# Kernel tuning notes

Measured on AMD Instinct MI355X. Metric: run time of the kernel, lower is better.

## Reference

```python
import jax, jax.numpy as jnp
import numpy as np

QMIN, QMAX = 0, 255        # 8-bit asymmetric activation quant bounds
GROUP_SIZE = 128

def setup_inputs() -> dict:
    key = jax.random.key(0)
    k1, k2, k3, k4, k5 = jax.random.split(key, 5)
    x = jax.random.normal(k1, (1, 2048, 4096), dtype=jnp.float32)
    qweight = jax.random.randint(k2, (4096, 32, 128), 0, 16, dtype=jnp.int32)  # uint4 codes
    w_scales = jax.random.uniform(k3, (4096, 32), dtype=jnp.float32, minval=0.001, maxval=0.02)
    w_zero_points = jax.random.randint(k4, (4096, 32), 0, 16, dtype=jnp.int32)
    bias = jax.random.normal(k5, (4096,), dtype=jnp.float32)
    return {"x": x, "qweight": qweight, "w_scales": w_scales,
            "w_zero_points": w_zero_points, "bias": bias}

def reference(x, qweight, w_scales, w_zero_points, bias):
    xf = x.astype(jnp.float32)
    # per-token (last-dim) asymmetric dynamic activation quantization
    xmin = jnp.min(xf, axis=-1, keepdims=True)
    xmax = jnp.max(xf, axis=-1, keepdims=True)
    x_scale = jnp.clip((xmax - xmin) / (QMAX - QMIN), 1e-5, None)
    x_zp = jnp.clip(jnp.round(-xmin / x_scale), QMIN, QMAX)
    q = jnp.clip(jnp.round(xf / x_scale) + x_zp, QMIN, QMAX)
    centered_x = (q - x_zp).reshape(*x.shape[:-1], -1, GROUP_SIZE)  # [B,S,G,C]
    # grouped weight dequant (zero-point centered)
    centered_w = qweight.astype(jnp.float32) - w_zero_points.astype(jnp.float32)[..., None]  # [O,G,C]
    acc = jnp.einsum('bsgc,ogc->bsog', centered_x, centered_w)  # [B,S,O,G]
    out = (acc * w_scales[None, None]).sum(axis=-1)  # apply per-group weight scales
    out = out * x_scale  # per-token activation scale
    out = out + bias
    return out
```

## Files before the change

### kernel.cpp

```cpp
#include <hip/hip_runtime.h>
#include <stdint.h>

#define M_DIM 2048
#define N_DIM 4096
#define K_DIM 4096
#define NGROUP 32
#define GSIZE 128

#define RQ_UP   (127.0f / 15.0f)
#define RQ_DOWN (15.0f / 127.0f)

#define BM 256
#define BN 128
#define KSLICE 64
#define NSLICE (K_DIM / KSLICE)
#define ASLOT (BM * KSLICE)
#define BSLOT (BN * KSLICE)

typedef __attribute__((ext_vector_type(4))) int int32x4_t;

static __device__ __forceinline__ void gl2lds16(const void* g, void* l) {
    auto gp = (const __attribute__((address_space(1))) unsigned int*)(uintptr_t)g;
    auto lp = (__attribute__((address_space(3))) unsigned int*)(uintptr_t)l;
    __builtin_amdgcn_global_load_lds(gp, lp, 16, 0, 0);
}

#define WAITVM_(N) asm volatile("s_waitcnt vmcnt(" #N ")" ::: "memory")
#define WAITVM(N) WAITVM_(N)
#define BARRIER() asm volatile("s_barrier" ::: "memory")

#define QUANT_BLOCKS M_DIM
#define DEQ_BLOCKS ((N_DIM * K_DIM) / 8 / 256)

__global__ __launch_bounds__(256) void prep_kernel(
        const float* __restrict__ x,
        const int* __restrict__ qw,
        const float* __restrict__ wsc,
        const int* __restrict__ wzp,
        char* __restrict__ A8,
        char* __restrict__ Bt8,
        float* __restrict__ xscale,
        float* __restrict__ xzpc,
        int* __restrict__ Sw)
{
    const int t = threadIdx.x;
    if (blockIdx.x < QUANT_BLOCKS) {
        const int s = blockIdx.x;
        const float* xrow = x + (size_t)s * K_DIM;

        float xv[16];
        float vmin = 1e38f, vmax = -1e38f;
#pragma unroll
        for (int p = 0; p < 4; ++p) {
            float4 v = *((const float4*)(xrow + p * 1024) + t);
            xv[p*4+0] = v.x; xv[p*4+1] = v.y; xv[p*4+2] = v.z; xv[p*4+3] = v.w;
            vmin = fminf(vmin, fminf(fminf(v.x, v.y), fminf(v.z, v.w)));
            vmax = fmaxf(vmax, fmaxf(fmaxf(v.x, v.y), fmaxf(v.z, v.w)));
        }
#pragma unroll
        for (int off = 32; off > 0; off >>= 1) {
            vmin = fminf(vmin, __shfl_xor(vmin, off));
            vmax = fmaxf(vmax, __shfl_xor(vmax, off));
        }
        __shared__ float smin[4], smax[4];
        const int wave = t >> 6;
        if ((t & 63) == 0) { smin[wave] = vmin; smax[wave] = vmax; }
        __syncthreads();
        vmin = fminf(fminf(smin[0], smin[1]), fminf(smin[2], smin[3]));
        vmax = fmaxf(fmaxf(smax[0], smax[1]), fmaxf(smax[2], smax[3]));

        float sc = (vmax - vmin) / 255.0f;
        sc = fmaxf(sc, 1e-5f);
        float zp = rintf(-vmin / sc);
        zp = fminf(fmaxf(zp, 0.0f), 255.0f);

#pragma unroll
        for (int p = 0; p < 4; ++p) {
            int b[4];
#pragma unroll
            for (int e = 0; e < 4; ++e) {
                float q = fminf(fmaxf(rintf(xv[p*4+e] / sc) + zp, 0.0f), 255.0f);
                b[e] = (int)q - 128;
            }
            unsigned pack = (b[0] & 0xff) | ((b[1] & 0xff) << 8) |
                            ((b[2] & 0xff) << 16) | ((b[3] & 0xff) << 24);
            *(unsigned*)(A8 + (size_t)s * K_DIM + p * 1024 + t * 4) = pack;
        }
        if (t == 0) { xscale[s] = sc; xzpc[s] = 128.0f - zp; }
    } else {
        const size_t base = ((size_t)(blockIdx.x - QUANT_BLOCKS) * 256 + t) * 8;
        const int n = (int)(base >> 12);
        const int g = (int)((base >> 7) & 31);
        const int zp = wzp[n * NGROUP + g];

        const int cl = t & 15;
        float2 wp = *(const float2*)(wsc + (size_t)n * NGROUP + cl * 2);
        float smx = fmaxf(wp.x, wp.y);
#pragma unroll
        for (int off = 1; off < 16; off <<= 1)
            smx = fmaxf(smx, __shfl_xor(smx, off));
        const float factor = wsc[n * NGROUP + g] * (RQ_UP / smx);

        int4 c0 = *(const int4*)(qw + base);
        int4 c1 = *(const int4*)(qw + base + 4);
        int w[8];
        w[0] = (int)rintf((float)(c0.x - zp) * factor);
        w[1] = (int)rintf((float)(c0.y - zp) * factor);
        w[2] = (int)rintf((float)(c0.z - zp) * factor);
        w[3] = (int)rintf((float)(c0.w - zp) * factor);
        w[4] = (int)rintf((float)(c1.x - zp) * factor);
        w[5] = (int)rintf((float)(c1.y - zp) * factor);
        w[6] = (int)rintf((float)(c1.z - zp) * factor);
        w[7] = (int)rintf((float)(c1.w - zp) * factor);
        uint2 pk;
        pk.x = (w[0] & 0xff) | ((w[1] & 0xff) << 8) | ((w[2] & 0xff) << 16) | ((w[3] & 0xff) << 24);
        pk.y = (w[4] & 0xff) | ((w[5] & 0xff) << 8) | ((w[6] & 0xff) << 16) | ((w[7] & 0xff) << 24);
        *(uint2*)(Bt8 + base) = pk;

        int s8 = w[0] + w[1] + w[2] + w[3] + w[4] + w[5] + w[6] + w[7];
#pragma unroll
        for (int off = 1; off < 16; off <<= 1) s8 += __shfl_xor(s8, off);
        if ((t & 15) == 0)
            Sw[n * NGROUP + g] = s8;
    }
}

__global__ __launch_bounds__(512, 2) void gemm_kernel(
        const char* __restrict__ A8,
        const char* __restrict__ Bt8,
        const float* __restrict__ xscale,
        const float* __restrict__ xzpc,
        const float* __restrict__ wsc,
        const int* __restrict__ Sw,
        const float* __restrict__ bias,
        float* __restrict__ out)
{
    __shared__ __align__(16) char As[4][ASLOT];
    __shared__ __align__(16) char Bs[4][BSLOT];
    __shared__ float fws_s[BN], wsf_s[BN];

    const int tid  = threadIdx.x;
    const int bn   = blockIdx.x;
    const int bm   = blockIdx.y;
    const int wave = tid >> 6;
    const int lane = tid & 63;
    const int wr   = wave >> 1;
    const int wcl  = wave & 1;
    const int lrow  = lane & 15;
    const int lquad = lane >> 4;

    if (tid < BN) {
        const int n = bn * BN + tid;
        const int4* s4 = (const int4*)(Sw + (size_t)n * NGROUP);
        int acc = 0;
#pragma unroll
        for (int p = 0; p < 8; ++p) { int4 v = s4[p]; acc += v.x + v.y + v.z + v.w; }
        const float4* w4 = (const float4*)(wsc + (size_t)n * NGROUP);
        float s = 0.f;
#pragma unroll
        for (int p = 0; p < 8; ++p) {
            float4 w = w4[p];
            s = fmaxf(s, fmaxf(fmaxf(w.x, w.y), fmaxf(w.z, w.w)));
        }
        const float fw = s * RQ_DOWN;
        fws_s[tid] = fw;
        wsf_s[tid] = fw * (float)acc;
    }
    asm volatile("s_waitcnt vmcnt(0) lgkmcnt(0)" ::: "memory");
    BARRIER();

    const char* Ab = A8  + (size_t)(bm * BM) * K_DIM;
    const char* Bb = Bt8 + (size_t)(bn * BN) * K_DIM;
    const int lsub = lane >> 2;
    const int csrc = (lane & 3) ^ ((lane >> 3) & 3);
    const char* gA0 = Ab + (size_t)((wave      ) * 16 + lsub) * K_DIM + csrc * 16;
    const char* gA1 = Ab + (size_t)((wave + 8  ) * 16 + lsub) * K_DIM + csrc * 16;
    const char* gB0 = Bb + (size_t)((wave      ) * 16 + lsub) * K_DIM + csrc * 16;
    const int lA0 = wave * 1024;
    const int lA1 = 8192 + wave * 1024;
    const int lB0 = wave * 1024;

    const int xq = (lquad ^ ((lrow >> 1) & 3)) * 16;
    int aoff[4], boff[4];
#pragma unroll
    for (int i = 0; i < 4; ++i)
        aoff[i] = (wr * 64 + i * 16 + lrow) * KSLICE + xq;
#pragma unroll
    for (int j = 0; j < 4; ++j)
        boff[j] = (wcl * 64 + j * 16 + lrow) * KSLICE + xq;

    int32x4_t iacc[4][4];
    const int32x4_t zi = {0, 0, 0, 0};
#pragma unroll
    for (int i = 0; i < 4; ++i)
#pragma unroll
        for (int j = 0; j < 4; ++j) iacc[i][j] = zi;

#define STAGE(t) {                                                   \
        const int sl_ = (t) & 3;                                     \
        const size_t k0_ = (size_t)(t) * KSLICE;                     \
        gl2lds16(gA0 + k0_, &As[sl_][0] + lA0);                      \
        gl2lds16(gA1 + k0_, &As[sl_][0] + lA1);                      \
        gl2lds16(gB0 + k0_, &Bs[sl_][0] + lB0);                      \
    }

#define SLICE(s, VMN) {                                              \
        if ((s) + 3 < NSLICE) STAGE((s) + 3);                        \
        WAITVM(VMN);                                                 \
        BARRIER();                                                   \
        const char* Ap_ = &As[(s) & 3][0];                           \
        const char* Bp_ = &Bs[(s) & 3][0];                           \
        int32x4_t af_[4], bf_[4];                                    \
        _Pragma("unroll")                                            \
        for (int i_ = 0; i_ < 4; ++i_)                               \
            af_[i_] = *(const int32x4_t*)(Ap_ + aoff[i_]);           \
        _Pragma("unroll")                                            \
        for (int j_ = 0; j_ < 4; ++j_)                               \
            bf_[j_] = *(const int32x4_t*)(Bp_ + boff[j_]);           \
        __builtin_amdgcn_s_setprio(1);                               \
        _Pragma("unroll")                                            \
        for (int i_ = 0; i_ < 4; ++i_)                               \
            _Pragma("unroll")                                        \
            for (int j_ = 0; j_ < 4; ++j_)                           \
                iacc[i_][j_] = __builtin_amdgcn_mfma_i32_16x16x64_i8(\
                    af_[i_], bf_[j_], iacc[i_][j_], 0, 0, 0);        \
        __builtin_amdgcn_s_setprio(0);                               \
        BARRIER();                                                   \
    }

    STAGE(0); STAGE(1); STAGE(2);

    for (int s = 0; s < NSLICE - 3; ++s)
        SLICE(s, 9);
    SLICE(NSLICE - 3, 6);
    SLICE(NSLICE - 2, 3);
    SLICE(NSLICE - 1, 0);

    float fn[4], wf[4], bb[4];
    int ncol[4];
#pragma unroll
    for (int j = 0; j < 4; ++j) {
        const int ncl = wcl * 64 + j * 16 + lrow;
        ncol[j] = bn * BN + ncl;
        fn[j] = fws_s[ncl];
        wf[j] = wsf_s[ncl];
        bb[j] = bias[ncol[j]];
    }
    const int m0 = bm * BM + wr * 64;
#pragma unroll
    for (int i = 0; i < 4; ++i) {
#pragma unroll
        for (int r = 0; r < 4; ++r) {
            const int m = m0 + i * 16 + lquad * 4 + r;
            const float xs  = xscale[m];
            const float czp = xzpc[m];
            float* orow = out + (size_t)m * N_DIM;
#pragma unroll
            for (int j = 0; j < 4; ++j)
                orow[ncol[j]] = xs * (fn[j] * (float)iacc[i][j][r] + czp * wf[j]) + bb[j];
        }
    }
#undef SLICE
#undef STAGE
}

extern "C" void kernel_launch(void* const* d_in, const int* in_sizes, int n_in,
                              void* d_out, int out_size, void* d_ws, size_t ws_size,
                              hipStream_t stream) {
    const float* x     = (const float*)d_in[0];
    const int*   qw    = (const int*)d_in[1];
    const float* wsc   = (const float*)d_in[2];
    const int*   wzp   = (const int*)d_in[3];
    const float* bias  = (const float*)d_in[4];
    float* out = (float*)d_out;

    char* A8  = (char*)d_ws;
    char* Bt8 = A8 + (size_t)M_DIM * K_DIM;
    float* xscale = (float*)(Bt8 + (size_t)N_DIM * K_DIM);
    float* xzpc   = xscale + M_DIM;
    int*   Sw     = (int*)(xzpc + M_DIM);

    prep_kernel<<<QUANT_BLOCKS + DEQ_BLOCKS, 256, 0, stream>>>(
        x, qw, wsc, wzp, A8, Bt8, xscale, xzpc, Sw);
    dim3 grid(N_DIM / BN, M_DIM / BM);
    gemm_kernel<<<grid, 512, 0, stream>>>(A8, Bt8, xscale, xzpc, wsc, Sw, bias, out);
}
```

Baseline: 173.8 us.

## Double-buffer LDS fragment reads to overlap with MFMAs, remap block order

The main loop is restructured so the LDS fragment reads for the next K-slice are issued before the MFMAs of the current slice, using two register fragment sets that alternate. A partial lgkmcnt wait and a sched_barrier keep the compiler from reordering across that point. Launch bounds change from 2 blocks per CU to 1, freeing registers for the extra fragments. The grid becomes 1D with bm taken as the fast index, so consecutive blocks share the same B tile for L2 reuse. The risk is lower occupancy and the reliance on a hand-set wait count.

```diff
diff --git a/kernel.cpp b/kernel.cpp
--- a/kernel.cpp
+++ b/kernel.cpp
@@ -27,6 +27,8 @@
 
 #define WAITVM_(N) asm volatile("s_waitcnt vmcnt(" #N ")" ::: "memory")
 #define WAITVM(N) WAITVM_(N)
+#define WAITLGKM_(N) asm volatile("s_waitcnt lgkmcnt(" #N ")" ::: "memory")
+#define WAITLGKM(N) WAITLGKM_(N)
 #define BARRIER() asm volatile("s_barrier" ::: "memory")
 
 #define QUANT_BLOCKS M_DIM
@@ -125,7 +127,7 @@
     }
 }
 
-__global__ __launch_bounds__(512, 2) void gemm_kernel(
+__global__ __launch_bounds__(512, 1) void gemm_kernel(
         const char* __restrict__ A8,
         const char* __restrict__ Bt8,
         const float* __restrict__ xscale,
@@ -140,8 +142,9 @@
     __shared__ float fws_s[BN], wsf_s[BN];
 
     const int tid  = threadIdx.x;
-    const int bn   = blockIdx.x;
-    const int bm   = blockIdx.y;
+    const int bid  = blockIdx.x;
+    const int bm   = bid & 7;
+    const int bn   = bid >> 3;
     const int wave = tid >> 6;
     const int lane = tid & 63;
     const int wr   = wave >> 1;
@@ -196,6 +199,8 @@
 #pragma unroll
         for (int j = 0; j < 4; ++j) iacc[i][j] = zi;
 
+    int32x4_t afA[4], bfA[4], afB[4], bfB[4];
+
 #define STAGE(t) {                                                   \
         const int sl_ = (t) & 3;                                     \
         const size_t k0_ = (size_t)(t) * KSLICE;                     \
@@ -204,37 +209,59 @@
         gl2lds16(gB0 + k0_, &Bs[sl_][0] + lB0);                      \
     }
 
-#define SLICE(s, VMN) {                                              \
-        if ((s) + 3 < NSLICE) STAGE((s) + 3);                        \
-        WAITVM(VMN);                                                 \
-        BARRIER();                                                   \
+#define READF(s, af, bf) {                                           \
         const char* Ap_ = &As[(s) & 3][0];                           \
         const char* Bp_ = &Bs[(s) & 3][0];                           \
-        int32x4_t af_[4], bf_[4];                                    \
         _Pragma("unroll")                                            \
         for (int i_ = 0; i_ < 4; ++i_)                               \
-            af_[i_] = *(const int32x4_t*)(Ap_ + aoff[i_]);           \
+            af[i_] = *(const int32x4_t*)(Ap_ + aoff[i_]);            \
         _Pragma("unroll")                                            \
         for (int j_ = 0; j_ < 4; ++j_)                               \
-            bf_[j_] = *(const int32x4_t*)(Bp_ + boff[j_]);           \
+            bf[j_] = *(const int32x4_t*)(Bp_ + boff[j_]);            \
+    }
+
+#define MFMAS(af, bf) {                                              \
         __builtin_amdgcn_s_setprio(1);                               \
         _Pragma("unroll")                                            \
         for (int i_ = 0; i_ < 4; ++i_)                               \
             _Pragma("unroll")                                        \
             for (int j_ = 0; j_ < 4; ++j_)                           \
                 iacc[i_][j_] = __builtin_amdgcn_mfma_i32_16x16x64_i8(\
-                    af_[i_], bf_[j_], iacc[i_][j_], 0, 0, 0);        \
+                    af[i_], bf[j_], iacc[i_][j_], 0, 0, 0);          \
         __builtin_amdgcn_s_setprio(0);                               \
+    }
+
+#define BODY(s, VMN, CA, CB, NA, NB) {                               \
+        if ((s) + 3 < NSLICE) STAGE((s) + 3);                        \
+        WAITVM(VMN);                                                 \
         BARRIER();                                                   \
+        READF((s) + 1, NA, NB);                                      \
+        WAITLGKM(8);                                                 \
+        __builtin_amdgcn_sched_barrier(0);                           \
+        MFMAS(CA, CB);                                               \
+        BARRIER();                                                   \
     }
 
     STAGE(0); STAGE(1); STAGE(2);
-
-    for (int s = 0; s < NSLICE - 3; ++s)
-        SLICE(s, 9);
-    SLICE(NSLICE - 3, 6);
-    SLICE(NSLICE - 2, 3);
-    SLICE(NSLICE - 1, 0);
+    WAITVM(6);
+    BARRIER();
+    READF(0, afA, bfA);
+
+    for (int s = 0; s < NSLICE - 4; s += 2) {
+        BODY(s,     6, afA, bfA, afB, bfB);
+        BODY(s + 1, 6, afB, bfB, afA, bfA);
+    }
+    BODY(60, 6, afA, bfA, afB, bfB);
+    BODY(61, 3, afB, bfB, afA, bfA);
+    WAITVM(0);
+    BARRIER();
+    READF(63, afB, bfB);
+    WAITLGKM(8);
+    __builtin_amdgcn_sched_barrier(0);
+    MFMAS(afA, bfA);
+    WAITLGKM(0);
+    __builtin_amdgcn_sched_barrier(0);
+    MFMAS(afB, bfB);
 
     float fn[4], wf[4], bb[4];
     int ncol[4];
@@ -260,7 +287,9 @@
                 orow[ncol[j]] = xs * (fn[j] * (float)iacc[i][j][r] + czp * wf[j]) + bb[j];
         }
     }
-#undef SLICE
+#undef BODY
+#undef MFMAS
+#undef READF
 #undef STAGE
 }
 
@@ -282,6 +311,5 @@
 
     prep_kernel<<<QUANT_BLOCKS + DEQ_BLOCKS, 256, 0, stream>>>(
         x, qw, wsc, wzp, A8, Bt8, xscale, xzpc, Sw);
-    dim3 grid(N_DIM / BN, M_DIM / BM);
-    gemm_kernel<<<grid, 512, 0, stream>>>(A8, Bt8, xscale, xzpc, wsc, Sw, bias, out);
+    gemm_kernel<<<256, 512, 0, stream>>>(A8, Bt8, xscale, xzpc, wsc, Sw, bias, out);
 }
```

Measured after the change: 169.6 us. -2.4%, faster.

## Load A fragments directly to registers, keep only B in LDS with software pipeline

Applied to the files above, without the earlier changes.

The int8 GEMM kernel stops staging the A tile through LDS. Each wave now loads its own A fragments straight from global memory into double-buffered registers two slices ahead, while B is still staged through a 4-slot LDS ring and read one slice ahead. Launch bounds drop from 2 to 1 block per SM to make room for the extra registers. The aim is to cut LDS traffic and footprint and overlap LDS reads with MFMAs, at the cost of lower occupancy, uncoalesced per-lane global loads for A, and redundant A loads across the two waves that share a row. The manual vmcnt/lgkmcnt counts are fragile and must match the issue order exactly.

```diff
diff --git a/kernel.cpp b/kernel.cpp
--- a/kernel.cpp
+++ b/kernel.cpp
@@ -14,7 +14,6 @@
 #define BN 128
 #define KSLICE 64
 #define NSLICE (K_DIM / KSLICE)
-#define ASLOT (BM * KSLICE)
 #define BSLOT (BN * KSLICE)
 
 typedef __attribute__((ext_vector_type(4))) int int32x4_t;
@@ -27,6 +26,8 @@
 
 #define WAITVM_(N) asm volatile("s_waitcnt vmcnt(" #N ")" ::: "memory")
 #define WAITVM(N) WAITVM_(N)
+#define WAITLGKM_(N) asm volatile("s_waitcnt lgkmcnt(" #N ")" ::: "memory")
+#define WAITLGKM(N) WAITLGKM_(N)
 #define BARRIER() asm volatile("s_barrier" ::: "memory")
 
 #define QUANT_BLOCKS M_DIM
@@ -125,7 +126,7 @@
     }
 }
 
-__global__ __launch_bounds__(512, 2) void gemm_kernel(
+__global__ __launch_bounds__(512, 1) void gemm_kernel(
         const char* __restrict__ A8,
         const char* __restrict__ Bt8,
         const float* __restrict__ xscale,
@@ -135,7 +136,6 @@
         const float* __restrict__ bias,
         float* __restrict__ out)
 {
-    __shared__ __align__(16) char As[4][ASLOT];
     __shared__ __align__(16) char Bs[4][BSLOT];
     __shared__ float fws_s[BN], wsf_s[BN];
 
@@ -167,24 +167,17 @@
         wsf_s[tid] = fw * (float)acc;
     }
     asm volatile("s_waitcnt vmcnt(0) lgkmcnt(0)" ::: "memory");
-    BARRIER();
-
-    const char* Ab = A8  + (size_t)(bm * BM) * K_DIM;
+
     const char* Bb = Bt8 + (size_t)(bn * BN) * K_DIM;
     const int lsub = lane >> 2;
     const int csrc = (lane & 3) ^ ((lane >> 3) & 3);
-    const char* gA0 = Ab + (size_t)((wave      ) * 16 + lsub) * K_DIM + csrc * 16;
-    const char* gA1 = Ab + (size_t)((wave + 8  ) * 16 + lsub) * K_DIM + csrc * 16;
-    const char* gB0 = Bb + (size_t)((wave      ) * 16 + lsub) * K_DIM + csrc * 16;
-    const int lA0 = wave * 1024;
-    const int lA1 = 8192 + wave * 1024;
+    const char* gB0 = Bb + (size_t)(wave * 16 + lsub) * K_DIM + csrc * 16;
     const int lB0 = wave * 1024;
 
+    const char* gA = A8 + (size_t)(bm * BM + wr * 64 + lrow) * K_DIM + lquad * 16;
+
     const int xq = (lquad ^ ((lrow >> 1) & 3)) * 16;
-    int aoff[4], boff[4];
-#pragma unroll
-    for (int i = 0; i < 4; ++i)
-        aoff[i] = (wr * 64 + i * 16 + lrow) * KSLICE + xq;
+    int boff[4];
 #pragma unroll
     for (int j = 0; j < 4; ++j)
         boff[j] = (wcl * 64 + j * 16 + lrow) * KSLICE + xq;
@@ -196,45 +189,69 @@
 #pragma unroll
         for (int j = 0; j < 4; ++j) iacc[i][j] = zi;
 
-#define STAGE(t) {                                                   \
-        const int sl_ = (t) & 3;                                     \
-        const size_t k0_ = (size_t)(t) * KSLICE;                     \
-        gl2lds16(gA0 + k0_, &As[sl_][0] + lA0);                      \
-        gl2lds16(gA1 + k0_, &As[sl_][0] + lA1);                      \
-        gl2lds16(gB0 + k0_, &Bs[sl_][0] + lB0);                      \
-    }
-
-#define SLICE(s, VMN) {                                              \
-        if ((s) + 3 < NSLICE) STAGE((s) + 3);                        \
-        WAITVM(VMN);                                                 \
-        BARRIER();                                                   \
-        const char* Ap_ = &As[(s) & 3][0];                           \
-        const char* Bp_ = &Bs[(s) & 3][0];                           \
-        int32x4_t af_[4], bf_[4];                                    \
-        _Pragma("unroll")                                            \
-        for (int i_ = 0; i_ < 4; ++i_)                               \
-            af_[i_] = *(const int32x4_t*)(Ap_ + aoff[i_]);           \
-        _Pragma("unroll")                                            \
-        for (int j_ = 0; j_ < 4; ++j_)                               \
-            bf_[j_] = *(const int32x4_t*)(Bp_ + boff[j_]);           \
-        __builtin_amdgcn_s_setprio(1);                               \
-        _Pragma("unroll")                                            \
-        for (int i_ = 0; i_ < 4; ++i_)                               \
-            _Pragma("unroll")                                        \
-            for (int j_ = 0; j_ < 4; ++j_)                           \
-                iacc[i_][j_] = __builtin_amdgcn_mfma_i32_16x16x64_i8(\
-                    af_[i_], bf_[j_], iacc[i_][j_], 0, 0, 0);        \
-        __builtin_amdgcn_s_setprio(0);                               \
-        BARRIER();                                                   \
-    }
-
-    STAGE(0); STAGE(1); STAGE(2);
-
-    for (int s = 0; s < NSLICE - 3; ++s)
-        SLICE(s, 9);
-    SLICE(NSLICE - 3, 6);
-    SLICE(NSLICE - 2, 3);
-    SLICE(NSLICE - 1, 0);
+    int32x4_t aX[4], aY[4], bX[4], bY[4];
+
+#define STAGEB(t) gl2lds16(gB0 + (size_t)(t) * KSLICE, &Bs[(t) & 3][0] + lB0)
+
+#define LOADA(t, ar) {                                                \
+        _Pragma("unroll")                                             \
+        for (int i_ = 0; i_ < 4; ++i_)                                \
+            ar[i_] = *(const int32x4_t*)(gA + (size_t)i_ * 16 * K_DIM \
+                                            + (size_t)(t) * KSLICE);  \
+    }
+
+#define READB(t, br) {                                                \
+        const char* Bp_ = &Bs[(t) & 3][0];                            \
+        _Pragma("unroll")                                             \
+        for (int j_ = 0; j_ < 4; ++j_)                                \
+            br[j_] = *(const int32x4_t*)(Bp_ + boff[j_]);             \
+    }
+
+#define MFMAS(ar, br) {                                               \
+        __builtin_amdgcn_s_setprio(1);                                \
+        _Pragma("unroll")                                             \
+        for (int i_ = 0; i_ < 4; ++i_)                                \
+            _Pragma("unroll")                                         \
+            for (int j_ = 0; j_ < 4; ++j_)                            \
+                iacc[i_][j_] = __builtin_amdgcn_mfma_i32_16x16x64_i8( \
+                    ar[i_], br[j_], iacc[i_][j_], 0, 0, 0);           \
+        __builtin_amdgcn_s_setprio(0);                                \
+    }
+
+#define BODY(s, VMN, AC, AN, BC, BNX) {                               \
+        if ((s) + 3 < NSLICE) STAGEB((s) + 3);                        \
+        WAITVM(VMN);                                                  \
+        BARRIER();                                                    \
+        READB((s) + 1, BNX);                                          \
+        WAITLGKM(4);                                                  \
+        __builtin_amdgcn_sched_barrier(0);                            \
+        MFMAS(AC, BC);                                                \
+        if ((s) + 2 < NSLICE) LOADA((s) + 2, AC);                     \
+    }
+
+    STAGEB(0); LOADA(0, aX);
+    STAGEB(1); LOADA(1, aY);
+    STAGEB(2);
+    WAITVM(10);
+    BARRIER();
+    READB(0, bX);
+
+    for (int s = 0; s < NSLICE - 4; s += 2) {
+        BODY(s,     6, aX, aY, bX, bY);
+        BODY(s + 1, 6, aY, aX, bY, bX);
+    }
+    BODY(60, 6, aX, aY, bX, bY);
+    BODY(61, 5, aY, aX, bY, bX);
+    WAITVM(4);
+    BARRIER();
+    READB(63, bY);
+    WAITLGKM(4);
+    __builtin_amdgcn_sched_barrier(0);
+    MFMAS(aX, bX);
+    WAITVM(0);
+    WAITLGKM(0);
+    __builtin_amdgcn_sched_barrier(0);
+    MFMAS(aY, bY);
 
     float fn[4], wf[4], bb[4];
     int ncol[4];
@@ -260,8 +277,11 @@
                 orow[ncol[j]] = xs * (fn[j] * (float)iacc[i][j][r] + czp * wf[j]) + bb[j];
         }
     }
-#undef SLICE
-#undef STAGE
+#undef BODY
+#undef MFMAS
+#undef READB
+#undef LOADA
+#undef STAGEB
 }
 
 extern "C" void kernel_launch(void* const* d_in, const int* in_sizes, int n_in,
```

Result: slower. 196.4 us (+13.0%).
